# Kernel optimization log

Hardware: AMD Instinct MI355X
Metric: run time of the kernel (lower is better)

## Reference

```python
import jax, jax.numpy as jnp
import numpy as np

N, D, H, DPE, WALK, L, E = 2048, 512, 8, 16, 8, 3, 32768
HD = D // H
DFF = 4 * D


def setup_inputs() -> dict:
    key = jax.random.key(0)
    ks = jax.random.split(key, 16)
    s = 0.02
    return {
        "node_features": jax.random.normal(ks[0], (N, D), jnp.float32),
        "edge_index": jax.random.randint(ks[1], (2, E), 0, N, dtype=jnp.int32),
        "pe_proj_W": jax.random.normal(ks[2], (WALK, DPE), jnp.float32) * s,
        "pe_proj_b": jnp.zeros((DPE,), jnp.float32),
        "qkv_W": jax.random.normal(ks[3], (L, D, 3 * D), jnp.float32) * s,
        "qkv_b": jnp.zeros((L, 3 * D), jnp.float32),
        "peb_W": jax.random.normal(ks[4], (L, DPE, H), jnp.float32) * s,
        "peb_b": jnp.zeros((L, H), jnp.float32),
        "out_W": jax.random.normal(ks[5], (L, D, D), jnp.float32) * s,
        "out_b": jnp.zeros((L, D), jnp.float32),
        "ffn_W1": jax.random.normal(ks[6], (L, D, DFF), jnp.float32) * s,
        "ffn_b1": jnp.zeros((L, DFF), jnp.float32),
        "ffn_W2": jax.random.normal(ks[7], (L, DFF, D), jnp.float32) * s,
        "ffn_b2": jnp.zeros((L, D), jnp.float32),
        "ln1_g": jnp.ones((L, D), jnp.float32),
        "ln1_b": jnp.zeros((L, D), jnp.float32),
        "ln2_g": jnp.ones((L, D), jnp.float32),
        "ln2_b": jnp.zeros((L, D), jnp.float32),
    }


def _layer_norm(x, g, b, eps=1e-5):
    mu = x.mean(-1, keepdims=True)
    var = ((x - mu) ** 2).mean(-1, keepdims=True)
    return (x - mu) * jax.lax.rsqrt(var + eps) * g + b


def _rw_pe(edge_index, pe_proj_W, pe_proj_b, dtype):
    src, tgt = edge_index[0], edge_index[1]
    adj = jnp.zeros((N, N), dtype).at[src, tgt].set(1.0).at[tgt, src].set(1.0)
    deg = jnp.maximum(adj.sum(axis=1, keepdims=True), 1.0)
    T = adj / deg  # row-stochastic transition matrix

    def step(Tk, _):
        return Tk @ T, jnp.diagonal(Tk)

    _, diags = jax.lax.scan(step, T, None, length=WALK)  # [WALK, N]
    rw = diags.T  # [N, WALK] k-step return probabilities
    return rw @ pe_proj_W + pe_proj_b  # [N, DPE]


def reference(node_features, edge_index, pe_proj_W, pe_proj_b, qkv_W, qkv_b,
              peb_W, peb_b, out_W, out_b, ffn_W1, ffn_b1, ffn_W2, ffn_b2,
              ln1_g, ln1_b, ln2_g, ln2_b):
    pe = _rw_pe(edge_index, pe_proj_W, pe_proj_b, node_features.dtype)
    scale = HD ** -0.5
    x = node_features
    for l in range(L):
        qkv = (x @ qkv_W[l] + qkv_b[l]).reshape(N, 3, H, HD)
        q = jnp.transpose(qkv[:, 0], (1, 0, 2))  # [H, N, HD]
        k = jnp.transpose(qkv[:, 1], (1, 0, 2))
        v = jnp.transpose(qkv[:, 2], (1, 0, 2))
        pe_p = pe @ peb_W[l] + peb_b[l]  # [N, H]
        # bias[h, i, j] = pe_p[i, h] - pe_p[j, h]
        bias = pe_p.T[:, :, None] - pe_p.T[:, None, :]
        scores = jnp.einsum('hnd,hmd->hnm', q, k) * scale + bias
        attn = jax.nn.softmax(scores, axis=-1)
        o = jnp.einsum('hnm,hmd->hnd', attn, v)
        o = jnp.transpose(o, (1, 0, 2)).reshape(N, D) @ out_W[l] + out_b[l]
        x = _layer_norm(x + o, ln1_g[l], ln1_b[l])
        h = jax.nn.gelu(x @ ffn_W1[l] + ffn_b1[l], approximate=False)
        h = h @ ffn_W2[l] + ffn_b2[l]
        x = _layer_norm(x + h, ln2_g[l], ln2_b[l])
    return x
```

## Files before the change

kernel.cpp:

```cpp
#include <hip/hip_runtime.h>
#include <cstdint>
#include <cstddef>

#define NN 2048
#define DM 512
#define NH 8
#define HD 64
#define NL 3
#define NE 32768

typedef unsigned short u16;
typedef unsigned int u32;
typedef __attribute__((ext_vector_type(8))) short short8;
typedef __attribute__((ext_vector_type(4))) float float4v;

__device__ __forceinline__ float bf2f(u16 s){
  union { unsigned u; float f; } v; v.u = ((unsigned)s) << 16; return v.f;
}
__device__ __forceinline__ u16 f2bf(float f){
  union { float f; unsigned u; } v; v.f = f;
  unsigned r = v.u + 0x7fffu + ((v.u >> 16) & 1u);
  return (u16)(r >> 16);
}
__device__ __forceinline__ u16 f2bf_fast(float f){
  union { float f; unsigned u; } v; v.f = f;
  return (u16)((v.u + 0x8000u) >> 16);
}
__device__ __forceinline__ void gl_lds16(const void* g, void* l){
  __builtin_amdgcn_global_load_lds((const __attribute__((address_space(1))) void*)g,
                                   (__attribute__((address_space(3))) void*)l, 16, 0, 0);
}

__global__ void adj_scatter(const int* __restrict__ ei, float* __restrict__ A){
  int e = blockIdx.x*256 + threadIdx.x;
  if (e < NE){
    int s = ei[e], t = ei[NE + e];
    A[(size_t)s*NN + t] = 1.f;
    A[(size_t)t*NN + s] = 1.f;
  }
}

__global__ __launch_bounds__(256)
void rowsum_dinv(const float* __restrict__ A, float* __restrict__ dinv){
  int row = blockIdx.x, tid = threadIdx.x;
  __shared__ float red[4];
  float s = 0.f;
  for (int j=tid;j<NN;j+=256) s += A[(size_t)row*NN + j];
  #pragma unroll
  for (int off=32;off>0;off>>=1) s += __shfl_down(s, off);
  if ((tid&63)==0) red[tid>>6] = s;
  __syncthreads();
  if (tid==0) dinv[row] = rsqrtf(fmaxf(red[0]+red[1]+red[2]+red[3], 1.f));
}

__global__ __launch_bounds__(256)
void build_s_nz(const float* __restrict__ A, const float* __restrict__ dinv,
                u16* __restrict__ S, u32* __restrict__ nz, int* __restrict__ cnt){
  const int i = blockIdx.x, tid = threadIdx.x;
  __shared__ int lc;
  if (tid==0) lc = 0;
  __syncthreads();
  const float di = dinv[i];
  for (int j=tid; j<NN; j+=256){
    float a = A[(size_t)i*NN + j];
    u16 v = f2bf(a * di * dinv[j]);
    S[(size_t)i*NN + j] = v;
    if (v){
      int s = atomicAdd(&lc, 1);
      if (s < 128) nz[i*128 + s] = ((u32)j << 16) | v;
    }
  }
  __syncthreads();
  if (tid==0) cnt[i] = lc < 128 ? lc : 128;
}

__global__ __launch_bounds__(256)
void spmm(const u16* __restrict__ Bold, const u32* __restrict__ nz,
          const int* __restrict__ cnt, u16* __restrict__ Bnew)
{
  const int j = blockIdx.x, tid = threadIdx.x;
  __shared__ u32 lnz[128];
  __shared__ int lcnt;
  if (tid==0) lcnt = cnt[j];
  if (tid<128) lnz[tid] = nz[j*128 + tid];
  __syncthreads();
  const int n = lcnt;
  float acc[8] = {0,0,0,0,0,0,0,0};
  for (int e=0; e<n; e++){
    u32 p = lnz[e];
    int k = p >> 16;
    float wv = bf2f((u16)(p & 0xffffu));
    short8 rv = *(const short8*)&Bold[(size_t)k*NN + tid*8];
    #pragma unroll
    for (int t=0;t<8;t++) acc[t] = fmaf(bf2f((u16)rv[t]), wv, acc[t]);
  }
  short8 o;
  #pragma unroll
  for (int t=0;t<8;t++) o[t] = (short)f2bf(acc[t]);
  *(short8*)&Bnew[(size_t)j*NN + tid*8] = o;
}

__global__ __launch_bounds__(256)
void diag_pe(const u16* __restrict__ S, const u16* __restrict__ S2,
             const u16* __restrict__ S3, const u16* __restrict__ S4,
             const float* __restrict__ peW, const float* __restrict__ peb,
             const float* __restrict__ pebW, const float* __restrict__ pebb,
             float* __restrict__ pebT)
{
  const int i = blockIdx.x, tid = threadIdx.x;
  float d[7] = {0,0,0,0,0,0,0};
  for (int j=tid;j<NN;j+=256){
    float s1 = bf2f(S [(size_t)i*NN + j]);
    float s2 = bf2f(S2[(size_t)i*NN + j]);
    float s3 = bf2f(S3[(size_t)i*NN + j]);
    float s4 = bf2f(S4[(size_t)i*NN + j]);
    d[0] += s1*s1; d[1] += s1*s2; d[2] += s2*s2; d[3] += s2*s3;
    d[4] += s3*s3; d[5] += s3*s4; d[6] += s4*s4;
  }
  __shared__ float red[28];
  __shared__ float pv[16];
  #pragma unroll
  for (int t=0;t<7;t++){
    float v = d[t];
    #pragma unroll
    for (int off=32;off>0;off>>=1) v += __shfl_down(v, off);
    if ((tid&63)==0) red[t*4 + (tid>>6)] = v;
  }
  __syncthreads();
  if (tid < 16){
    float rr[8];
    rr[0] = bf2f(S[(size_t)i*NN + i]);
    #pragma unroll
    for (int t=0;t<7;t++) rr[t+1] = red[t*4]+red[t*4+1]+red[t*4+2]+red[t*4+3];
    float a = peb[tid];
    #pragma unroll
    for (int k=0;k<8;k++) a += rr[k]*peW[k*16 + tid];
    pv[tid] = a;
  }
  __syncthreads();
  if (tid < 24){
    int l = tid >> 3, h = tid & 7;
    float a = pebb[l*NH + h];
    #pragma unroll
    for (int p=0;p<16;p++) a += pv[p]*pebW[(l*16+p)*NH + h];
    pebT[((size_t)l*NH + h)*NN + i] = a;
  }
}

__global__ void init_x(const float* __restrict__ nf, float* __restrict__ x, u16* __restrict__ xbf){
  size_t i = (size_t)blockIdx.x*256 + threadIdx.x;
  float v = nf[i]; x[i] = v; xbf[i] = f2bf(v);
}

__global__ __launch_bounds__(256)
void transpose_all(const float* __restrict__ qkvW, const float* __restrict__ outW,
                   const float* __restrict__ f1W,  const float* __restrict__ f2W,
                   u16* __restrict__ qkvT, u16* __restrict__ outT,
                   u16* __restrict__ f1T,  u16* __restrict__ f2T)
{
  __shared__ float t[32][33];
  int gid = blockIdx.x;
  int l = gid / 3072, r = gid % 3072;
  const float* W; u16* WT; int K, N, bx, by;
  if (r < 768)      { W=qkvW; WT=qkvT; K=512;  N=1536; bx=r%48;        by=r/48; }
  else if (r < 1024){ int u=r-768;  W=outW; WT=outT; K=512;  N=512;  bx=u%16; by=u/16; }
  else if (r < 2048){ int u=r-1024; W=f1W;  WT=f1T;  K=512;  N=2048; bx=u%64; by=u/64; }
  else              { int u=r-2048; W=f2W;  WT=f2T;  K=2048; N=512;  bx=u%16; by=u/16; }
  W  += (size_t)l*K*N;
  WT += (size_t)l*K*N;
  int n0 = bx*32, k0 = by*32;
  int tx = threadIdx.x & 31, ty = threadIdx.x >> 5;
  #pragma unroll
  for (int i=0;i<32;i+=8) t[ty+i][tx] = W[(size_t)(k0+ty+i)*N + n0+tx];
  __syncthreads();
  #pragma unroll
  for (int i=0;i<32;i+=8) WT[(size_t)(n0+ty+i)*K + k0+tx] = f2bf(t[tx][ty+i]);
}

__global__ __launch_bounds__(256)
void ln_kernel(const float* __restrict__ xin, const float* __restrict__ add, int nsl,
               const float* __restrict__ g, const float* __restrict__ b,
               float* __restrict__ xout, u16* __restrict__ xbf)
{
  const int row = blockIdx.x, tid = threadIdx.x;
  __shared__ float red[8];
  const size_t base = (size_t)row*DM;
  float v0 = xin[base+tid];
  float v1 = xin[base+256+tid];
  for (int s=0;s<nsl;s++){
    v0 += add[(size_t)s*NN*DM + base+tid];
    v1 += add[(size_t)s*NN*DM + base+256+tid];
  }
  float s = v0+v1, sq = v0*v0 + v1*v1;
  #pragma unroll
  for (int off=32; off>0; off>>=1){ s += __shfl_down(s, off); sq += __shfl_down(sq, off); }
  if ((tid&63)==0){ red[tid>>6] = s; red[4+(tid>>6)] = sq; }
  __syncthreads();
  float mean = (red[0]+red[1]+red[2]+red[3]) * (1.f/512.f);
  float var  = (red[4]+red[5]+red[6]+red[7]) * (1.f/512.f) - mean*mean;
  float rstd = rsqrtf(var + 1e-5f);
  float y0 = (v0-mean)*rstd*g[tid]     + b[tid];
  float y1 = (v1-mean)*rstd*g[256+tid] + b[256+tid];
  xout[base+tid] = y0;     xout[base+256+tid] = y1;
  xbf[base+tid]  = f2bf(y0); xbf[base+256+tid] = f2bf(y1);
}

template<int OUTMODE, int GELU, int BIAS>
__global__ __launch_bounds__(256)
void gemm64(const u16* __restrict__ A, const u16* __restrict__ BT,
            const float* __restrict__ bias, void* __restrict__ Cout,
            int M, int N, int K, int ldc, int kper)
{
  __shared__ u16 As[64*32];
  __shared__ u16 Bs[64*32];
  const int tid = threadIdx.x, lane = tid & 63, wave = tid >> 6;
  const int q = lane >> 4, lo = lane & 15;
  const int bm = blockIdx.y, bn = blockIdx.x;
  const int wm = wave >> 1, wn = wave & 1;
  const int k_begin = blockIdx.z * kper, k_end = k_begin + kper;
  const int lrow  = lane >> 2;
  const int lkoff = (lane & 3) * 8;

  const u16* Ag = A  + ((size_t)bm*64 + 16*wave + lrow) * (size_t)K;
  const u16* Bg = BT + ((size_t)bn*64 + 16*wave + lrow) * (size_t)K;
  u16* AsW = As + (16*wave)*32;
  u16* BsW = Bs + (16*wave)*32;

  float4v acc[2][2] = {};

  for (int k0 = k_begin; k0 < k_end; k0 += 32){
    __syncthreads();
    gl_lds16(Ag + k0 + lkoff, AsW);
    gl_lds16(Bg + k0 + lkoff, BsW);
    __syncthreads();
    const short8* Ar = (const short8*)As;
    const short8* Br = (const short8*)Bs;
    short8 af[2], bfr[2];
    #pragma unroll
    for (int mt=0;mt<2;mt++) af[mt]  = Ar[(32*wm + 16*mt + lo)*4 + q];
    #pragma unroll
    for (int nt=0;nt<2;nt++) bfr[nt] = Br[(32*wn + 16*nt + lo)*4 + q];
    #pragma unroll
    for (int mt=0;mt<2;mt++)
      #pragma unroll
      for (int nt=0;nt<2;nt++)
        acc[mt][nt] = __builtin_amdgcn_mfma_f32_16x16x32_bf16(af[mt], bfr[nt], acc[mt][nt], 0, 0, 0);
  }

  float* Cf = (float*)Cout;
  u16*   Cb = (u16*)Cout;
  const size_t zoff = (OUTMODE == 2) ? (size_t)blockIdx.z * M * ldc : 0;
  #pragma unroll
  for (int mt=0;mt<2;mt++){
    const int row = bm*64 + 32*wm + 16*mt + q*4;
    #pragma unroll
    for (int nt=0;nt<2;nt++){
      const int col = bn*64 + 32*wn + 16*nt + lo;
      float bbc = (BIAS==1) ? bias[col] : 0.f;
      #pragma unroll
      for (int r=0;r<4;r++){
        float v = acc[mt][nt][r];
        float bb = (BIAS==2) ? bias[row+r] : bbc;
        if (OUTMODE == 2){
          if (BIAS && blockIdx.z == 0) v += bb;
          Cf[zoff + (size_t)(row+r)*ldc + col] = v;
        } else {
          v += bb;
          if (GELU) v = 0.5f*v*(1.f + erff(v*0.70710678118654752f));
          if (OUTMODE == 1) Cb[(size_t)(row+r)*ldc + col] = f2bf(v);
          else              Cf[(size_t)(row+r)*ldc + col] = v;
        }
      }
    }
  }
}

__global__ __launch_bounds__(256)
void attn_part(const u16* __restrict__ qkB, const u16* __restrict__ vT,
               const float* __restrict__ pebT, float* __restrict__ Opart,
               float* __restrict__ Lsum)
{
  __shared__ u16 Ks[64*72];
  __shared__ u16 Vs[64*72];
  __shared__ u16 Ps[128*72];
  __shared__ float CB[64];
  const int tid = threadIdx.x, lane = tid&63, wave = tid>>6;
  const int q = lane>>4, lo = lane&15;
  const int qb = blockIdx.x, h = blockIdx.y, ks = blockIdx.z;
  const int i0 = qb*128;
  const int part = (ks*NH + h)*16 + qb;

  short8 qf[2][2];
  #pragma unroll
  for (int mt=0;mt<2;mt++)
    #pragma unroll
    for (int kk=0;kk<2;kk++)
      qf[kk][mt] = *(const short8*)&qkB[(size_t)(i0 + 32*wave + 16*mt + lo)*1024 + h*64 + kk*32 + q*8];

  float l_r[2][4] = {};
  float4v o_acc[2][4] = {};

  const int j_begin = ks*512, j_end = j_begin + 512;
  for (int j0 = j_begin; j0 < j_end; j0 += 64){
    __syncthreads();
    for (int c = tid; c < 512; c += 256){
      int row = c >> 3, off = c & 7;
      *(float4v*)&Ks[row*72 + off*8] =
        *(const float4v*)&qkB[(size_t)(j0+row)*1024 + 512 + h*64 + off*8];
      *(float4v*)&Vs[row*72 + off*8] =
        *(const float4v*)&vT[(size_t)(h*64+row)*NN + j0 + off*8];
    }
    if (tid < 64) CB[tid] = pebT[(size_t)h*NN + j0 + tid] * 1.4426950408889634f;
    __syncthreads();

    float4v sacc[2][4] = {};
    const short8* Kr = (const short8*)Ks;
    #pragma unroll
    for (int kk=0; kk<2; kk++){
      #pragma unroll
      for (int nt=0; nt<4; nt++){
        short8 bfr = Kr[(16*nt + lo)*9 + kk*4 + q];
        #pragma unroll
        for (int mt=0; mt<2; mt++)
          sacc[mt][nt] = __builtin_amdgcn_mfma_f32_16x16x32_bf16(qf[kk][mt], bfr, sacc[mt][nt], 0,0,0);
      }
    }
    #pragma unroll
    for (int mt=0; mt<2; mt++)
      #pragma unroll
      for (int nt=0; nt<4; nt++){
        float cb = CB[16*nt + lo];
        #pragma unroll
        for (int r=0;r<4;r++){
          float p = exp2f(fmaf(sacc[mt][nt][r], 0.180336880f, -cb));
          l_r[mt][r] += p;
          Ps[(32*wave + 16*mt + q*4 + r)*72 + 16*nt + lo] = f2bf_fast(p);
        }
      }
    const short8* Pr = (const short8*)Ps;
    const short8* Vr = (const short8*)Vs;
    #pragma unroll
    for (int kk=0;kk<2;kk++){
      #pragma unroll
      for (int mt=0;mt<2;mt++){
        short8 af = Pr[(32*wave + 16*mt + lo)*9 + kk*4 + q];
        #pragma unroll
        for (int nt=0;nt<4;nt++){
          short8 bfr = Vr[(16*nt + lo)*9 + kk*4 + q];
          o_acc[mt][nt] = __builtin_amdgcn_mfma_f32_16x16x32_bf16(af, bfr, o_acc[mt][nt], 0,0,0);
        }
      }
    }
  }
  float* Op = Opart + (size_t)part*8192;
  #pragma unroll
  for (int mt=0;mt<2;mt++){
    #pragma unroll
    for (int r=0;r<4;r++){
      float s = l_r[mt][r];
      s += __shfl_xor(s, 1);
      s += __shfl_xor(s, 2);
      s += __shfl_xor(s, 4);
      s += __shfl_xor(s, 8);
      if (lo == 0) Lsum[part*128 + 32*wave + 16*mt + q*4 + r] = s;
    }
    #pragma unroll
    for (int nt=0;nt<4;nt++)
      #pragma unroll
      for (int r=0;r<4;r++)
        Op[(32*wave + 16*mt + q*4 + r)*64 + 16*nt + lo] = o_acc[mt][nt][r];
  }
}

__global__ __launch_bounds__(256)
void attn_combine(const float* __restrict__ Opart, const float* __restrict__ Lsum,
                  u16* __restrict__ obuf)
{
  const int qb = blockIdx.x, h = blockIdx.y, tid = threadIdx.x;
  __shared__ float invL[128];
  if (tid < 128){
    float L = 0.f;
    #pragma unroll
    for (int k=0;k<4;k++) L += Lsum[((k*NH + h)*16 + qb)*128 + tid];
    invL[tid] = 1.f / L;
  }
  __syncthreads();
  const int col = tid & 63, r0 = (tid >> 6) * 32;
  #pragma unroll
  for (int r=0;r<32;r++){
    int row = r0 + r;
    float acc = 0.f;
    #pragma unroll
    for (int k=0;k<4;k++)
      acc += Opart[((size_t)((k*NH + h)*16 + qb))*8192 + row*64 + col];
    obuf[(size_t)(qb*128 + row)*DM + h*64 + col] = f2bf(acc * invL[row]);
  }
}

extern "C" void kernel_launch(void* const* d_in, const int* in_sizes, int n_in,
                              void* d_out, int out_size, void* d_ws, size_t ws_size,
                              hipStream_t stream) {
  const float* nf   = (const float*)d_in[0];
  const int*   ei   = (const int*)d_in[1];
  const float* peW  = (const float*)d_in[2];
  const float* peb  = (const float*)d_in[3];
  const float* qkvW = (const float*)d_in[4];
  const float* qkvb = (const float*)d_in[5];
  const float* pebW = (const float*)d_in[6];
  const float* pebb = (const float*)d_in[7];
  const float* outW = (const float*)d_in[8];
  const float* outb = (const float*)d_in[9];
  const float* f1W  = (const float*)d_in[10];
  const float* f1b  = (const float*)d_in[11];
  const float* f2W  = (const float*)d_in[12];
  const float* f2b  = (const float*)d_in[13];
  const float* ln1g = (const float*)d_in[14];
  const float* ln1b = (const float*)d_in[15];
  const float* ln2g = (const float*)d_in[16];
  const float* ln2b = (const float*)d_in[17];
  (void)in_sizes; (void)n_in; (void)out_size; (void)ws_size;

  char* w = (char*)d_ws;
  constexpr size_t OFF_A     = 0;
  constexpr size_t OFF_S     = OFF_A + 16777216;
  constexpr size_t OFF_S2    = OFF_S + 8388608;
  constexpr size_t OFF_S3    = OFF_S2 + 8388608;
  constexpr size_t OFF_S4    = OFF_S3 + 8388608;
  constexpr size_t OFF_DINV  = OFF_S4 + 8388608;
  constexpr size_t OFF_PEBT  = OFF_DINV + 8192;
  constexpr size_t OFF_QKVT  = OFF_PEBT + 196608;
  constexpr size_t OFF_OUTT  = OFF_QKVT + 4718592;
  constexpr size_t OFF_F1T   = OFF_OUTT + 1572864;
  constexpr size_t OFF_F2T   = OFF_F1T + 6291456;
  constexpr size_t OFF_X     = OFF_F2T + 6291456;
  constexpr size_t OFF_XBF   = OFF_X + 4194304;
  constexpr size_t OFF_QKB   = OFF_XBF + 2097152;
  constexpr size_t OFF_VT    = OFF_QKB + 4194304;
  constexpr size_t OFF_OBUF  = OFF_VT + 2097152;
  constexpr size_t OFF_NZ    = OFF_OBUF + 2097152;
  constexpr size_t OFF_CNT   = OFF_NZ + 1048576;
  constexpr size_t OFF_LS    = OFF_CNT + 8192;
  constexpr size_t OFF_HBUF  = OFF_LS + 262144;

  float* A     = (float*)(w + OFF_A);
  u16*   S     = (u16*)  (w + OFF_S);
  u16*   S2    = (u16*)  (w + OFF_S2);
  u16*   S3    = (u16*)  (w + OFF_S3);
  u16*   S4    = (u16*)  (w + OFF_S4);
  float* dinv  = (float*)(w + OFF_DINV);
  float* pebT  = (float*)(w + OFF_PEBT);
  u16*   qkvT  = (u16*)  (w + OFF_QKVT);
  u16*   outT  = (u16*)  (w + OFF_OUTT);
  u16*   f1T   = (u16*)  (w + OFF_F1T);
  u16*   f2T   = (u16*)  (w + OFF_F2T);
  float* x     = (float*)(w + OFF_X);
  u16*   xbf   = (u16*)  (w + OFF_XBF);
  u16*   qkB   = (u16*)  (w + OFF_QKB);
  u16*   vT    = (u16*)  (w + OFF_VT);
  u16*   obuf  = (u16*)  (w + OFF_OBUF);
  u32*   NZ    = (u32*)  (w + OFF_NZ);
  int*   CNT   = (int*)  (w + OFF_CNT);
  float* Lsum  = (float*)(w + OFF_LS);
  u16*   hbuf  = (u16*)  (w + OFF_HBUF);
  float* Opart = A;

  hipMemsetAsync(A, 0, 16777216, stream);
  adj_scatter<<<dim3(NE/256), 256, 0, stream>>>(ei, A);
  rowsum_dinv<<<dim3(NN), 256, 0, stream>>>(A, dinv);
  build_s_nz<<<dim3(NN), 256, 0, stream>>>(A, dinv, S, NZ, CNT);
  spmm<<<dim3(NN), 256, 0, stream>>>(S,  NZ, CNT, S2);
  spmm<<<dim3(NN), 256, 0, stream>>>(S2, NZ, CNT, S3);
  spmm<<<dim3(NN), 256, 0, stream>>>(S3, NZ, CNT, S4);
  diag_pe<<<dim3(NN), 256, 0, stream>>>(S, S2, S3, S4, peW, peb, pebW, pebb, pebT);

  transpose_all<<<dim3(9216), 256, 0, stream>>>(qkvW, outW, f1W, f2W, qkvT, outT, f1T, f2T);
  init_x<<<dim3(NN*DM/256), 256, 0, stream>>>(nf, x, xbf);

  for (int l = 0; l < NL; l++){
    gemm64<1,0,1><<<dim3(16,32,1), 256, 0, stream>>>(
        xbf, qkvT + (size_t)l*1536*512, qkvb + l*1536, qkB, 2048, 1024, 512, 1024, 512);
    gemm64<1,0,2><<<dim3(32,8,1), 256, 0, stream>>>(
        qkvT + (size_t)l*1536*512 + (size_t)1024*512, xbf, qkvb + l*1536 + 1024, vT,
        512, 2048, 512, 2048, 512);
    attn_part<<<dim3(16,8,4), 256, 0, stream>>>(qkB, vT, pebT + (size_t)l*NH*NN, Opart, Lsum);
    attn_combine<<<dim3(16,8), 256, 0, stream>>>(Opart, Lsum, obuf);

    gemm64<2,0,1><<<dim3(8,32,2), 256, 0, stream>>>(
        obuf, outT + (size_t)l*512*512, outb + l*512, A, 2048, 512, 512, 512, 256);
    ln_kernel<<<dim3(NN), 256, 0, stream>>>(x, A, 2, ln1g + l*512, ln1b + l*512, x, xbf);

    gemm64<1,1,1><<<dim3(32,32,1), 256, 0, stream>>>(
        xbf, f1T + (size_t)l*2048*512, f1b + l*2048, hbuf, 2048, 2048, 512, 2048, 512);
    gemm64<2,0,1><<<dim3(8,32,4), 256, 0, stream>>>(
        hbuf, f2T + (size_t)l*512*2048, f2b + l*512, A, 2048, 512, 2048, 512, 512);
    float* xout = (l == NL-1) ? (float*)d_out : x;
    ln_kernel<<<dim3(NN), 256, 0, stream>>>(x, A, 4, ln2g + l*512, ln2b + l*512, xout, xbf);
  }
}
```

Before: 511.7 us.

## Double-buffer GEMM and attention tiles, fuse QKV launches, sparse-square first walk step

The GEMM body now double-buffers its LDS tiles, issuing the next K-slice load before computing on the current one, and the attention kernel prefetches the next K/V/bias tile into registers and stores it into a second LDS buffer after the MFMAs. The QK and V projection GEMMs are merged into one launch that dispatches on block id. The first random-walk power step is computed as a sparse-by-sparse product, accumulating into a shared-memory row with LDS atomics, instead of reading the dense S. The aim is to hide global-load latency, cut one launch per layer, and drop dense reads in the PE precompute, at the cost of doubled LDS use, which may lower occupancy, and atomic contention in the sparse product.

```diff
diff --git a/kernel.cpp b/kernel.cpp
--- a/kernel.cpp
+++ b/kernel.cpp
@@ -72,6 +72,37 @@
   }
   __syncthreads();
   if (tid==0) cnt[i] = lc < 128 ? lc : 128;
+}
+
+__global__ __launch_bounds__(256)
+void spmm_sq(const u32* __restrict__ nz, const int* __restrict__ cnt,
+             u16* __restrict__ S2)
+{
+  const int j = blockIdx.x, tid = threadIdx.x;
+  __shared__ float row[2048];
+  __shared__ u32 lnz[128];
+  __shared__ int lcnt;
+  for (int c=tid;c<2048;c+=256) row[c] = 0.f;
+  if (tid==0) lcnt = cnt[j];
+  if (tid<128) lnz[tid] = nz[j*128 + tid];
+  __syncthreads();
+  const int n = lcnt;
+  const int g = tid >> 3, sub = tid & 7;
+  for (int e = g; e < n; e += 32){
+    u32 p = lnz[e];
+    int k = p >> 16;
+    float wv = bf2f((u16)(p & 0xffffu));
+    int m = cnt[k];
+    for (int f = sub; f < m; f += 8){
+      u32 qq = nz[k*128 + f];
+      atomicAdd(&row[qq >> 16], wv * bf2f((u16)(qq & 0xffffu)));
+    }
+  }
+  __syncthreads();
+  short8 o;
+  #pragma unroll
+  for (int t=0;t<8;t++) o[t] = (short)f2bf(row[tid*8 + t]);
+  *(short8*)&S2[(size_t)j*NN + tid*8] = o;
 }
 
 __global__ __launch_bounds__(256)
@@ -206,35 +237,38 @@
 }
 
 template<int OUTMODE, int GELU, int BIAS>
-__global__ __launch_bounds__(256)
-void gemm64(const u16* __restrict__ A, const u16* __restrict__ BT,
-            const float* __restrict__ bias, void* __restrict__ Cout,
-            int M, int N, int K, int ldc, int kper)
-{
-  __shared__ u16 As[64*32];
-  __shared__ u16 Bs[64*32];
+__device__ __forceinline__ void gemm_body(
+    u16* As, u16* Bs,
+    const u16* __restrict__ A, const u16* __restrict__ BT,
+    const float* __restrict__ bias, void* __restrict__ Cout,
+    int M, int N, int K, int ldc, int kper, int bm, int bn, int bz)
+{
   const int tid = threadIdx.x, lane = tid & 63, wave = tid >> 6;
   const int q = lane >> 4, lo = lane & 15;
-  const int bm = blockIdx.y, bn = blockIdx.x;
   const int wm = wave >> 1, wn = wave & 1;
-  const int k_begin = blockIdx.z * kper, k_end = k_begin + kper;
+  const int k_begin = bz * kper;
   const int lrow  = lane >> 2;
   const int lkoff = (lane & 3) * 8;
-
-  const u16* Ag = A  + ((size_t)bm*64 + 16*wave + lrow) * (size_t)K;
-  const u16* Bg = BT + ((size_t)bn*64 + 16*wave + lrow) * (size_t)K;
-  u16* AsW = As + (16*wave)*32;
-  u16* BsW = Bs + (16*wave)*32;
+  const int woff = (16*wave)*32;
+
+  const u16* Ag = A  + ((size_t)bm*64 + 16*wave + lrow) * (size_t)K + lkoff + k_begin;
+  const u16* Bg = BT + ((size_t)bn*64 + 16*wave + lrow) * (size_t)K + lkoff + k_begin;
 
   float4v acc[2][2] = {};
-
-  for (int k0 = k_begin; k0 < k_end; k0 += 32){
+  const int kiters = kper >> 5;
+
+  gl_lds16(Ag, As + woff);
+  gl_lds16(Bg, Bs + woff);
+
+  for (int it = 0; it < kiters; ++it){
+    const int cur = (it & 1) << 11, nxt = cur ^ 2048;
     __syncthreads();
-    gl_lds16(Ag + k0 + lkoff, AsW);
-    gl_lds16(Bg + k0 + lkoff, BsW);
-    __syncthreads();
-    const short8* Ar = (const short8*)As;
-    const short8* Br = (const short8*)Bs;
+    if (it + 1 < kiters){
+      gl_lds16(Ag + (it+1)*32, As + nxt + woff);
+      gl_lds16(Bg + (it+1)*32, Bs + nxt + woff);
+    }
+    const short8* Ar = (const short8*)(As + cur);
+    const short8* Br = (const short8*)(Bs + cur);
     short8 af[2], bfr[2];
     #pragma unroll
     for (int mt=0;mt<2;mt++) af[mt]  = Ar[(32*wm + 16*mt + lo)*4 + q];
@@ -249,7 +283,7 @@
 
   float* Cf = (float*)Cout;
   u16*   Cb = (u16*)Cout;
-  const size_t zoff = (OUTMODE == 2) ? (size_t)blockIdx.z * M * ldc : 0;
+  const size_t zoff = (OUTMODE == 2) ? (size_t)bz * M * ldc : 0;
   #pragma unroll
   for (int mt=0;mt<2;mt++){
     const int row = bm*64 + 32*wm + 16*mt + q*4;
@@ -262,7 +296,7 @@
         float v = acc[mt][nt][r];
         float bb = (BIAS==2) ? bias[row+r] : bbc;
         if (OUTMODE == 2){
-          if (BIAS && blockIdx.z == 0) v += bb;
+          if (BIAS && bz == 0) v += bb;
           Cf[zoff + (size_t)(row+r)*ldc + col] = v;
         } else {
           v += bb;
@@ -275,15 +309,46 @@
   }
 }
 
+template<int OUTMODE, int GELU, int BIAS>
+__global__ __launch_bounds__(256)
+void gemm64(const u16* __restrict__ A, const u16* __restrict__ BT,
+            const float* __restrict__ bias, void* __restrict__ Cout,
+            int M, int N, int K, int ldc, int kper)
+{
+  __shared__ u16 As[2*2048];
+  __shared__ u16 Bs[2*2048];
+  gemm_body<OUTMODE,GELU,BIAS>(As, Bs, A, BT, bias, Cout, M, N, K, ldc, kper,
+                               blockIdx.y, blockIdx.x, blockIdx.z);
+}
+
+__global__ __launch_bounds__(256)
+void qkvt_fused(const u16* __restrict__ xbf, const u16* __restrict__ qkT,
+                const float* __restrict__ qkb, u16* __restrict__ qkB,
+                const u16* __restrict__ vwT, const float* __restrict__ vb,
+                u16* __restrict__ vT)
+{
+  __shared__ u16 As[2*2048];
+  __shared__ u16 Bs[2*2048];
+  int id = blockIdx.x;
+  if (id < 512)
+    gemm_body<1,0,1>(As, Bs, xbf, qkT, qkb, qkB, 2048, 1024, 512, 1024, 512,
+                     id >> 4, id & 15, 0);
+  else {
+    id -= 512;
+    gemm_body<1,0,2>(As, Bs, vwT, xbf, vb, vT, 512, 2048, 512, 2048, 512,
+                     id >> 5, id & 31, 0);
+  }
+}
+
 __global__ __launch_bounds__(256)
 void attn_part(const u16* __restrict__ qkB, const u16* __restrict__ vT,
                const float* __restrict__ pebT, float* __restrict__ Opart,
                float* __restrict__ Lsum)
 {
-  __shared__ u16 Ks[64*72];
-  __shared__ u16 Vs[64*72];
+  __shared__ u16 Ks[2][64*72];
+  __shared__ u16 Vs[2][64*72];
   __shared__ u16 Ps[128*72];
-  __shared__ float CB[64];
+  __shared__ float CB[2][64];
   const int tid = threadIdx.x, lane = tid&63, wave = tid>>6;
   const int q = lane>>4, lo = lane&15;
   const int qb = blockIdx.x, h = blockIdx.y, ks = blockIdx.z;
@@ -300,21 +365,36 @@
   float l_r[2][4] = {};
   float4v o_acc[2][4] = {};
 
+  const int srow = tid >> 2, soff = (tid & 3) * 16;
   const int j_begin = ks*512, j_end = j_begin + 512;
+
+  {
+    float4v k0a = *(const float4v*)&qkB[(size_t)(j_begin+srow)*1024 + 512 + h*64 + soff];
+    float4v k0b = *(const float4v*)&qkB[(size_t)(j_begin+srow)*1024 + 512 + h*64 + soff + 8];
+    float4v v0a = *(const float4v*)&vT[(size_t)(h*64+srow)*NN + j_begin + soff];
+    float4v v0b = *(const float4v*)&vT[(size_t)(h*64+srow)*NN + j_begin + soff + 8];
+    *(float4v*)&Ks[0][srow*72 + soff]     = k0a;
+    *(float4v*)&Ks[0][srow*72 + soff + 8] = k0b;
+    *(float4v*)&Vs[0][srow*72 + soff]     = v0a;
+    *(float4v*)&Vs[0][srow*72 + soff + 8] = v0b;
+    if (tid < 64) CB[0][tid] = pebT[(size_t)h*NN + j_begin + tid] * 1.4426950408889634f;
+  }
+  __syncthreads();
+
   for (int j0 = j_begin; j0 < j_end; j0 += 64){
-    __syncthreads();
-    for (int c = tid; c < 512; c += 256){
-      int row = c >> 3, off = c & 7;
-      *(float4v*)&Ks[row*72 + off*8] =
-        *(const float4v*)&qkB[(size_t)(j0+row)*1024 + 512 + h*64 + off*8];
-      *(float4v*)&Vs[row*72 + off*8] =
-        *(const float4v*)&vT[(size_t)(h*64+row)*NN + j0 + off*8];
-    }
-    if (tid < 64) CB[tid] = pebT[(size_t)h*NN + j0 + tid] * 1.4426950408889634f;
-    __syncthreads();
+    const int cur = ((j0 - j_begin) >> 6) & 1, nxt = cur ^ 1;
+    const bool has_next = (j0 + 64 < j_end);
+    float4v ka, kb, va, vb; float cbr = 0.f;
+    if (has_next){
+      ka = *(const float4v*)&qkB[(size_t)(j0+64+srow)*1024 + 512 + h*64 + soff];
+      kb = *(const float4v*)&qkB[(size_t)(j0+64+srow)*1024 + 512 + h*64 + soff + 8];
+      va = *(const float4v*)&vT[(size_t)(h*64+srow)*NN + j0+64 + soff];
+      vb = *(const float4v*)&vT[(size_t)(h*64+srow)*NN + j0+64 + soff + 8];
+      if (tid < 64) cbr = pebT[(size_t)h*NN + j0+64 + tid] * 1.4426950408889634f;
+    }
 
     float4v sacc[2][4] = {};
-    const short8* Kr = (const short8*)Ks;
+    const short8* Kr = (const short8*)Ks[cur];
     #pragma unroll
     for (int kk=0; kk<2; kk++){
       #pragma unroll
@@ -329,7 +409,7 @@
     for (int mt=0; mt<2; mt++)
       #pragma unroll
       for (int nt=0; nt<4; nt++){
-        float cb = CB[16*nt + lo];
+        float cb = CB[cur][16*nt + lo];
         #pragma unroll
         for (int r=0;r<4;r++){
           float p = exp2f(fmaf(sacc[mt][nt][r], 0.180336880f, -cb));
@@ -338,7 +418,7 @@
         }
       }
     const short8* Pr = (const short8*)Ps;
-    const short8* Vr = (const short8*)Vs;
+    const short8* Vr = (const short8*)Vs[cur];
     #pragma unroll
     for (int kk=0;kk<2;kk++){
       #pragma unroll
@@ -351,7 +431,16 @@
         }
       }
     }
-  }
+    if (has_next){
+      *(float4v*)&Ks[nxt][srow*72 + soff]     = ka;
+      *(float4v*)&Ks[nxt][srow*72 + soff + 8] = kb;
+      *(float4v*)&Vs[nxt][srow*72 + soff]     = va;
+      *(float4v*)&Vs[nxt][srow*72 + soff + 8] = vb;
+      if (tid < 64) CB[nxt][tid] = cbr;
+    }
+    __syncthreads();
+  }
+
   float* Op = Opart + (size_t)part*8192;
   #pragma unroll
   for (int mt=0;mt<2;mt++){
@@ -468,7 +557,7 @@
   adj_scatter<<<dim3(NE/256), 256, 0, stream>>>(ei, A);
   rowsum_dinv<<<dim3(NN), 256, 0, stream>>>(A, dinv);
   build_s_nz<<<dim3(NN), 256, 0, stream>>>(A, dinv, S, NZ, CNT);
-  spmm<<<dim3(NN), 256, 0, stream>>>(S,  NZ, CNT, S2);
+  spmm_sq<<<dim3(NN), 256, 0, stream>>>(NZ, CNT, S2);
   spmm<<<dim3(NN), 256, 0, stream>>>(S2, NZ, CNT, S3);
   spmm<<<dim3(NN), 256, 0, stream>>>(S3, NZ, CNT, S4);
   diag_pe<<<dim3(NN), 256, 0, stream>>>(S, S2, S3, S4, peW, peb, pebW, pebb, pebT);
@@ -477,11 +566,9 @@
   init_x<<<dim3(NN*DM/256), 256, 0, stream>>>(nf, x, xbf);
 
   for (int l = 0; l < NL; l++){
-    gemm64<1,0,1><<<dim3(16,32,1), 256, 0, stream>>>(
-        xbf, qkvT + (size_t)l*1536*512, qkvb + l*1536, qkB, 2048, 1024, 512, 1024, 512);
-    gemm64<1,0,2><<<dim3(32,8,1), 256, 0, stream>>>(
-        qkvT + (size_t)l*1536*512 + (size_t)1024*512, xbf, qkvb + l*1536 + 1024, vT,
-        512, 2048, 512, 2048, 512);
+    qkvt_fused<<<dim3(768), 256, 0, stream>>>(
+        xbf, qkvT + (size_t)l*1536*512, qkvb + l*1536, qkB,
+        qkvT + (size_t)l*1536*512 + (size_t)1024*512, qkvb + l*1536 + 1024, vT);
     attn_part<<<dim3(16,8,4), 256, 0, stream>>>(qkB, vT, pebT + (size_t)l*NH*NN, Opart, Lsum);
     attn_combine<<<dim3(16,8), 256, 0, stream>>>(Opart, Lsum, obuf);
 
```

Result: faster. 475.0 us (-7.2%).
